# Kernel optimization log

Hardware: AMD Instinct MI355X
Metric: run time of the kernel (lower is better)

Reference implementation:

```python
import math
import jax, jax.numpy as jnp
import numpy as np

D_MODEL = 896
N_HEADS = 14
D_HEAD = D_MODEL // N_HEADS  # 64
ROPE_BASE = 10000.0
LN_EPS = 1e-5
B, N = 8, 1024


def setup_inputs() -> dict:
    key = jax.random.key(0)
    ks = jax.random.split(key, 12)
    s = 1.0 / math.sqrt(D_MODEL)
    return {
        "node_features": jax.random.normal(ks[0], (B, N, D_MODEL), jnp.float32),
        "adj": jax.random.uniform(ks[1], (N, N), jnp.float32),
        "wind_dirs": jax.random.uniform(ks[2], (B, N), jnp.float32),
        "bearings": jax.random.uniform(ks[3], (N, N), jnp.float32),
        "Wq": jax.random.normal(ks[4], (D_MODEL, D_MODEL), jnp.float32) * s,
        "Wk": jax.random.normal(ks[5], (D_MODEL, D_MODEL), jnp.float32) * s,
        "Wv": jax.random.normal(ks[6], (D_MODEL, D_MODEL), jnp.float32) * s,
        "Wo": jax.random.normal(ks[7], (D_MODEL, D_MODEL), jnp.float32) * s,
        "ln_g": jnp.ones((D_MODEL,), jnp.float32),
        "ln_b": jnp.zeros((D_MODEL,), jnp.float32),
        "wind_w": jax.random.normal(ks[8], (2, N_HEADS), jnp.float32) * (1.0 / math.sqrt(2.0)),
        "wind_b": jnp.zeros((N_HEADS,), jnp.float32),
    }


def _layernorm(x, g, b):
    mu = jnp.mean(x, axis=-1, keepdims=True)
    var = jnp.var(x, axis=-1, keepdims=True)
    return (x - mu) * jax.lax.rsqrt(var + LN_EPS) * g + b


def _apply_rotary(x, cos_h, sin_h):
    # x: (B,H,N,d_head); cos_h/sin_h: (N, d_head//2)
    d_half = x.shape[-1] // 2
    x1, x2 = x[..., :d_half], x[..., d_half:]
    return jnp.concatenate([x1 * cos_h - x2 * sin_h, x2 * cos_h + x1 * sin_h], axis=-1)


def reference(node_features, adj, wind_dirs, bearings, Wq, Wk, Wv, Wo, ln_g, ln_b, wind_w, wind_b):
    Bb, Nn, D = node_features.shape
    residual = node_features
    x = _layernorm(node_features, ln_g, ln_b)

    def proj(W):
        return (x @ W).reshape(Bb, Nn, N_HEADS, D_HEAD).transpose(0, 2, 1, 3)  # (B,H,N,dh)

    Q, K, V = proj(Wq), proj(Wk), proj(Wv)

    # RoPE: cos/sin halves (first d_half entries of the duplicated freq table)
    inv_freq = 1.0 / (ROPE_BASE ** (jnp.arange(0, D_HEAD, 2, dtype=jnp.float32) / D_HEAD))
    freqs = jnp.arange(Nn, dtype=jnp.float32)[:, None] * inv_freq[None, :]  # (N, dh/2)
    cos_h, sin_h = jnp.cos(freqs), jnp.sin(freqs)
    Q = _apply_rotary(Q, cos_h, sin_h)
    K = _apply_rotary(K, cos_h, sin_h)

    attn = jnp.einsum("bhqd,bhkd->bhqk", Q, K) / math.sqrt(D_HEAD)
    adj_mask = (adj > 0)[None, None, :, :]
    attn = jnp.where(adj_mask, attn, -1e30)

    # wind-direction dynamic edge bias
    reverse_bearings = (bearings.T + 180.0) % 360.0  # (N,N)
    alignment = jnp.cos(jnp.deg2rad(wind_dirs[:, :, None] - reverse_bearings[None]))  # (B,N,N)
    dist_feat = jnp.broadcast_to(adj[None], (Bb, Nn, Nn))
    edge_features = jnp.stack([alignment, dist_feat], axis=-1)  # (B,N,N,2)
    wind_bias = jnp.tanh(edge_features @ wind_w + wind_b)  # (B,N,N,H)
    attn = attn + wind_bias.transpose(0, 3, 1, 2)  # (B,H,N,N)

    attn = jax.nn.softmax(attn, axis=-1)  # dropout is identity in eval
    out = jnp.einsum("bhqk,bhkd->bhqd", attn, V)
    out = out.transpose(0, 2, 1, 3).reshape(Bb, Nn, D) @ Wo
    return residual + out
```

## Files before the change

kernel.cpp:

```cpp
#include <hip/hip_runtime.h>
#include <hip/hip_bf16.h>
#include <math.h>

#define B_ 8
#define N_ 1024
#define H_ 14
#define DH_ 64
#define D_ 896
#define M_ (B_*N_)
#define DQKV_ 2688

#define TWO_LOG2E_ 2.8853900817779268f
#define BIAS_C_   (-15.869645449778597f)
#define QSCALE_     0.18033688011112043f

typedef __attribute__((ext_vector_type(8))) short bf16x8;
typedef __attribute__((ext_vector_type(4))) short bf16x4;
typedef __attribute__((ext_vector_type(4))) float f32x4;
typedef __attribute__((ext_vector_type(4))) unsigned u32x4;

__device__ __forceinline__ float bf2f(short s){
  unsigned u = ((unsigned)(unsigned short)s) << 16;
  union { unsigned u; float f; } c; c.u = u; return c.f;
}
__device__ __forceinline__ short f2bf(float f){
  union { float f; unsigned u; } c; c.f = f;
  unsigned u = c.u;
  unsigned r = (u + 0x7FFFu + ((u >> 16) & 1u)) >> 16;
  return (short)(unsigned short)r;
}
__device__ __forceinline__ float asf(unsigned u){
  union { unsigned u; float f; } c; c.u = u; return c.f;
}

#define BAR_LDS() do { asm volatile("s_waitcnt lgkmcnt(0)" ::: "memory"); \
                       __builtin_amdgcn_s_barrier(); } while (0)

__global__ __launch_bounds__(256) void ln_kernel(const float* __restrict__ x,
                                                 const float* __restrict__ g,
                                                 const float* __restrict__ bb,
                                                 short* __restrict__ y)
{
  int row = blockIdx.x;
  const float* xr = x + (size_t)row * D_;
  float s = 0.f, s2 = 0.f;
  for (int i = threadIdx.x; i < D_; i += 256){
    float v = xr[i]; s += v; s2 = fmaf(v, v, s2);
  }
  #pragma unroll
  for (int off = 32; off > 0; off >>= 1){
    s  += __shfl_down(s,  off, 64);
    s2 += __shfl_down(s2, off, 64);
  }
  __shared__ float rs_[4], rs2_[4];
  int wv = threadIdx.x >> 6;
  if ((threadIdx.x & 63) == 0){ rs_[wv] = s; rs2_[wv] = s2; }
  __syncthreads();
  float ts  = rs_[0] + rs_[1] + rs_[2] + rs_[3];
  float ts2 = rs2_[0] + rs2_[1] + rs2_[2] + rs2_[3];
  float mu  = ts * (1.f / D_);
  float var = ts2 * (1.f / D_) - mu * mu;
  float rstd = rsqrtf(var + 1e-5f);
  short* yr = y + (size_t)row * D_;
  for (int i = threadIdx.x; i < D_; i += 256){
    yr[i] = f2bf((xr[i] - mu) * rstd * g[i] + bb[i]);
  }
}

__global__ __launch_bounds__(256) void transpose_kernel(
    const float* __restrict__ Wq, const float* __restrict__ Wk,
    const float* __restrict__ Wv, const float* __restrict__ Wo,
    short* __restrict__ WqkvT, short* __restrict__ WoT)
{
  __shared__ short t[64][72];
  int z = blockIdx.z;
  const float* W = (z == 0) ? Wq : (z == 1) ? Wk : (z == 2) ? Wv : Wo;
  int kb = blockIdx.x * 64, nb = blockIdx.y * 64;
  int c0 = (threadIdx.x & 7) * 8;
  int r0 = threadIdx.x >> 3;
  #pragma unroll
  for (int rr = 0; rr < 64; rr += 32){
    const float* src = &W[(size_t)(kb + r0 + rr) * D_ + nb + c0];
    float4 a = *(const float4*)src;
    float4 b = *(const float4*)(src + 4);
    short* dstl = &t[r0 + rr][c0];
    dstl[0] = f2bf(a.x); dstl[1] = f2bf(a.y); dstl[2] = f2bf(a.z); dstl[3] = f2bf(a.w);
    dstl[4] = f2bf(b.x); dstl[5] = f2bf(b.y); dstl[6] = f2bf(b.z); dstl[7] = f2bf(b.w);
  }
  __syncthreads();
  short* dst = (z < 3) ? (WqkvT + (size_t)(z * D_) * D_) : WoT;
  #pragma unroll
  for (int rr = 0; rr < 64; rr += 32){
    int n = nb + r0 + rr;
    bf16x8 v;
    #pragma unroll
    for (int j = 0; j < 8; j++) v[j] = t[c0 + j][r0 + rr];
    *(bf16x8*)&dst[(size_t)n * D_ + kb + c0] = v;
  }
}

__global__ __launch_bounds__(256) void prep_kernel(
    const float* __restrict__ adj, const float* __restrict__ brg,
    const float* __restrict__ wdir,
    unsigned* __restrict__ csb, short* __restrict__ adjT,
    short* __restrict__ alignT, int do_align)
{
  int kt = blockIdx.x, qt = blockIdx.y;
  __shared__ short tt[64][72];
  __shared__ float cA_[8][64], sA_[8][64];

  if (do_align){
    for (int idx = threadIdx.x; idx < 8 * 64; idx += 256){
      int b = idx >> 6, q = idx & 63;
      float A = wdir[(size_t)b * N_ + qt * 64 + q] * 0.017453292519943295f;
      float s, c; __sincosf(A, &s, &c);
      sA_[b][q] = s; cA_[b][q] = c;
    }
  }

  int r  = threadIdx.x >> 2;
  int c0 = (threadIdx.x & 3) * 16;

  {
    int q = qt * 64 + r;
    const float* ap = adj + (size_t)q * N_ + kt * 64 + c0;
    #pragma unroll
    for (int i = 0; i < 16; i += 4){
      float4 av = *(const float4*)(ap + i);
      tt[r][c0 + i]     = f2bf(av.x);
      tt[r][c0 + i + 1] = f2bf(av.y);
      tt[r][c0 + i + 2] = f2bf(av.z);
      tt[r][c0 + i + 3] = f2bf(av.w);
    }
  }
  __syncthreads();

  {
    int k = kt * 64 + r;
    const float* bp = brg + (size_t)k * N_ + qt * 64 + c0;
    unsigned* cp = csb + (size_t)k * N_ + qt * 64 + c0;
    #pragma unroll
    for (int i = 0; i < 16; i += 4){
      float4 bv = *(const float4*)(bp + i);
      float b4[4] = { bv.x, bv.y, bv.z, bv.w };
      float cB[4], sB[4];
      unsigned o[4];
      #pragma unroll
      for (int j = 0; j < 4; j++){
        float Br = (b4[j] + 180.f) * 0.017453292519943295f;
        __sincosf(Br, &sB[j], &cB[j]);
        o[j] = ((unsigned)(unsigned short)f2bf(cB[j])) |
               (((unsigned)(unsigned short)f2bf(sB[j])) << 16);
      }
      *(uint4*)(cp + i) = make_uint4(o[0], o[1], o[2], o[3]);
      if (do_align){
        #pragma unroll
        for (int b = 0; b < 8; b++){
          unsigned w2[2];
          #pragma unroll
          for (int p = 0; p < 2; p++){
            unsigned lo = 0, hi = 0;
            #pragma unroll
            for (int j = 0; j < 2; j++){
              int q = c0 + i + p * 2 + j;
              float al = fmaf(cA_[b][q], cB[p * 2 + j], sA_[b][q] * sB[p * 2 + j]);
              unsigned v = (unsigned)(unsigned short)f2bf(al);
              if (j == 0) lo = v; else hi = v;
            }
            w2[p] = lo | (hi << 16);
          }
          *(uint2*)(alignT + ((size_t)b * N_ + k) * N_ + qt * 64 + c0 + i) =
              make_uint2(w2[0], w2[1]);
        }
      }
    }
  }

  {
    int k = kt * 64 + r;
    short* op = adjT + (size_t)k * N_ + qt * 64 + c0;
    bf16x8 v0, v1;
    #pragma unroll
    for (int j = 0; j < 8; j++){ v0[j] = tt[c0 + j][r]; v1[j] = tt[c0 + 8 + j][r]; }
    *(bf16x8*)op = v0;
    *(bf16x8*)(op + 8) = v1;
  }
}

__global__ __launch_bounds__(256) void gemm_bt(const short* __restrict__ A,
                                               const short* __restrict__ Bt,
                                               short* __restrict__ C,
                                               float* __restrict__ Cf,
                                               const float* __restrict__ residf,
                                               int N, int rope)
{
  const int K = D_;
  __shared__ short As[128 * 32];
  __shared__ short Bs[128 * 32];
  int tid  = threadIdx.x;
  int wave = tid >> 6;
  int lane = tid & 63;
  int quad = lane >> 4;
  int l16  = lane & 15;
  int wr = wave >> 1, wc = wave & 1;
  int m0 = blockIdx.x * 128;
  int n0 = blockIdx.y * 128;

  f32x4 acc[4][4];
  #pragma unroll
  for (int i = 0; i < 4; i++)
    #pragma unroll
    for (int j = 0; j < 4; j++)
      acc[i][j] = (f32x4){0.f, 0.f, 0.f, 0.f};

  for (int k0 = 0; k0 < K; k0 += 32){
    __syncthreads();
    #pragma unroll
    for (int it = 0; it < 2; ++it){
      int c   = tid + it * 256;
      int row = c >> 2;
      int cc  = c & 3;
      const short* ga = A  + (size_t)(m0 + row) * K + k0 + cc * 8;
      const short* gb = Bt + (size_t)(n0 + row) * K + k0 + cc * 8;
      short* la = As + (size_t)(wave * 64 + it * 256) * 8;
      short* lb = Bs + (size_t)(wave * 64 + it * 256) * 8;
      __builtin_amdgcn_global_load_lds((const __attribute__((address_space(1))) void*)ga,
                                       (__attribute__((address_space(3))) void*)la, 16, 0, 0);
      __builtin_amdgcn_global_load_lds((const __attribute__((address_space(1))) void*)gb,
                                       (__attribute__((address_space(3))) void*)lb, 16, 0, 0);
    }
    __syncthreads();

    bf16x8 af[4], bfr[4];
    #pragma unroll
    for (int i = 0; i < 4; i++)
      af[i] = *(const bf16x8*)(As + (size_t)(wr * 64 + i * 16 + l16) * 32 + quad * 8);
    #pragma unroll
    for (int j = 0; j < 4; j++)
      bfr[j] = *(const bf16x8*)(Bs + (size_t)(wc * 64 + j * 16 + l16) * 32 + quad * 8);
    #pragma unroll
    for (int i = 0; i < 4; i++)
      #pragma unroll
      for (int j = 0; j < 4; j++)
        acc[i][j] = __builtin_amdgcn_mfma_f32_16x16x32_bf16(af[i], bfr[j], acc[i][j], 0, 0, 0);
  }

  if (rope){
    int cb  = n0 + wc * 64;
    int mat = cb / D_;
    if (mat < 2){
      float scale = (mat == 0) ? QSCALE_ : 1.0f;
      float invf0 = exp2f(-0.4152410118609203f * (float)l16);
      float invf1 = invf0 * 0.01f;
      #pragma unroll
      for (int i = 0; i < 4; i++){
        #pragma unroll
        for (int rr = 0; rr < 4; rr++){
          int r = m0 + wr * 64 + i * 16 + quad * 4 + rr;
          float nseq = (float)(r & (N_ - 1));
          float s0, c0v, s1, c1v;
          __sincosf(nseq * invf0, &s0, &c0v);
          __sincosf(nseq * invf1, &s1, &c1v);
          float x1 = acc[i][0][rr], x2 = acc[i][2][rr];
          acc[i][0][rr] = (x1 * c0v - x2 * s0) * scale;
          acc[i][2][rr] = (x2 * c0v + x1 * s0) * scale;
          x1 = acc[i][1][rr]; x2 = acc[i][3][rr];
          acc[i][1][rr] = (x1 * c1v - x2 * s1) * scale;
          acc[i][3][rr] = (x2 * c1v + x1 * s1) * scale;
        }
      }
    }
  }

  #pragma unroll
  for (int i = 0; i < 4; i++){
    #pragma unroll
    for (int rr = 0; rr < 4; rr++){
      int r = m0 + wr * 64 + i * 16 + quad * 4 + rr;
      size_t rowoff = (size_t)r * N;
      #pragma unroll
      for (int j = 0; j < 4; j++){
        int cidx = n0 + wc * 64 + j * 16 + l16;
        float v = acc[i][j][rr];
        if (Cf){
          Cf[rowoff + cidx] = v + residf[rowoff + cidx];
        } else {
          C[rowoff + cidx] = f2bf(v);
        }
      }
    }
  }
}

template<int PRE>
__global__ __launch_bounds__(512, 4) void attn_kernel(
    const short* __restrict__ QKV,
    const unsigned* __restrict__ csb,
    const short* __restrict__ adjT,
    const short* __restrict__ alignT,
    const float* __restrict__ wind_dirs,
    const float* __restrict__ wind_w,
    const float* __restrict__ wind_b,
    short* __restrict__ outb)
{
  __shared__ short K_s[64 * 72];
  __shared__ short V_t[64 * 76];
  __shared__ short P_s[128 * 76];

  int bid = blockIdx.x;
  int qt  = bid & 7;
  int hh  = (bid >> 3) % H_;
  int b   = bid / (8 * H_);
  int q0  = qt * 128;

  int t    = threadIdx.x;
  int w    = t >> 6;
  int lane = t & 63;
  int quad = lane >> 4;
  int l16  = lane & 15;

  const short* qp = QKV + ((size_t)(b * N_) + q0 + w * 16 + l16) * DQKV_ + hh * DH_;
  bf16x8 qf0 = *(const bf16x8*)(qp + quad * 8);
  bf16x8 qf1 = *(const bf16x8*)(qp + 32 + quad * 8);

  float cA[4], sA[4];
  if (!PRE){
    #pragma unroll
    for (int rr = 0; rr < 4; rr++){
      float wd = wind_dirs[(size_t)b * N_ + q0 + w * 16 + quad * 4 + rr];
      float A  = wd * 0.017453292519943295f;
      sA[rr] = __sinf(A);
      cA[rr] = __cosf(A);
    }
  }
  float w0m = wind_w[hh]      * TWO_LOG2E_;
  float w1m = wind_w[H_ + hh] * TWO_LOG2E_;
  float wbm = wind_b[hh]      * TWO_LOG2E_;

  float l[4] = {0.f, 0.f, 0.f, 0.f};
  f32x4 O[4];
  #pragma unroll
  for (int dc = 0; dc < 4; dc++) O[dc] = (f32x4){0.f, 0.f, 0.f, 0.f};

  int kr  = t >> 3, kc8 = (t & 7) * 8;
  int vk2 = (t >> 4) * 2, vd4 = (t & 15) * 4;
  const short* kg0 = QKV + ((size_t)(b * N_) + kr)  * DQKV_ + D_     + hh * DH_ + kc8;
  const short* vg0 = QKV + ((size_t)(b * N_) + vk2) * DQKV_ + 2 * D_ + hh * DH_ + vd4;

  bf16x8 pk  = *(const bf16x8*)kg0;
  bf16x4 pv0 = *(const bf16x4*)vg0;
  bf16x4 pv1 = *(const bf16x4*)(vg0 + DQKV_);

  size_t bias_q = (size_t)(q0 + w * 16 + quad * 4);
  u32x4 cs4a[4]; bf16x4 al4a[4]; bf16x4 av4a[4];
  #pragma unroll
  for (int jc = 0; jc < 4; jc++){
    size_t off = (size_t)(jc * 16 + l16) * N_ + bias_q;
    if (PRE) al4a[jc] = *(const bf16x4*)(alignT + (size_t)b * N_ * N_ + off);
    else     cs4a[jc] = *(const u32x4*)(csb + off);
    av4a[jc] = *(const bf16x4*)(adjT + off);
  }

  for (int kt = 0; kt < 16; ++kt){
    int k0 = kt * 64;
    BAR_LDS();
    *(bf16x8*)(K_s + kr * 72 + kc8) = pk;
    #pragma unroll
    for (int j = 0; j < 4; j++){
      unsigned pv = ((unsigned)(unsigned short)pv0[j]) |
                    (((unsigned)(unsigned short)pv1[j]) << 16);
      *(unsigned*)(V_t + (vd4 + j) * 76 + vk2) = pv;
    }
    BAR_LDS();

    int kn = (kt < 15) ? (k0 + 64) : k0;
    pk  = *(const bf16x8*)(kg0 + (size_t)kn * DQKV_);
    pv0 = *(const bf16x4*)(vg0 + (size_t)kn * DQKV_);
    pv1 = *(const bf16x4*)(vg0 + (size_t)(kn + 1) * DQKV_);

    f32x4 S[4];
    __builtin_amdgcn_s_setprio(1);
    #pragma unroll
    for (int jc = 0; jc < 4; jc++){
      S[jc] = (f32x4){0.f, 0.f, 0.f, 0.f};
      bf16x8 kf0 = *(const bf16x8*)(K_s + (jc * 16 + l16) * 72 + quad * 8);
      bf16x8 kf1 = *(const bf16x8*)(K_s + (jc * 16 + l16) * 72 + 32 + quad * 8);
      S[jc] = __builtin_amdgcn_mfma_f32_16x16x32_bf16(qf0, kf0, S[jc], 0, 0, 0);
      S[jc] = __builtin_amdgcn_mfma_f32_16x16x32_bf16(qf1, kf1, S[jc], 0, 0, 0);
    }
    __builtin_amdgcn_s_setprio(0);

    #pragma unroll
    for (int jc = 0; jc < 4; jc++){
      #pragma unroll
      for (int rr = 0; rr < 4; rr++){
        float av = bf2f(av4a[jc][rr]);
        float align;
        if (PRE){
          align = bf2f(al4a[jc][rr]);
        } else {
          unsigned u = cs4a[jc][rr];
          float cB = asf(u << 16);
          float sB = asf(u & 0xffff0000u);
          align = cA[rr] * cB + sA[rr] * sB;
        }
        float z2 = fmaf(align, w0m, fmaf(av, w1m, wbm));
        float e2 = __builtin_amdgcn_exp2f(z2);
        float rc = __builtin_amdgcn_rcpf(e2 + 1.f);
        float bias2 = fmaf(-TWO_LOG2E_, rc, BIAS_C_);
        float sv = (av > 0.f ? S[jc][rr] : -1e30f) + bias2;
        float e = __builtin_amdgcn_exp2f(sv);
        l[rr] += e;
        P_s[(w * 16 + quad * 4 + rr) * 76 + jc * 16 + l16] = f2bf(e);
      }
    }

    #pragma unroll
    for (int jc = 0; jc < 4; jc++){
      size_t off = (size_t)(kn + jc * 16 + l16) * N_ + bias_q;
      if (PRE) al4a[jc] = *(const bf16x4*)(alignT + (size_t)b * N_ * N_ + off);
      else     cs4a[jc] = *(const u32x4*)(csb + off);
      av4a[jc] = *(const bf16x4*)(adjT + off);
    }

    __builtin_amdgcn_s_setprio(1);
    #pragma unroll
    for (int kc = 0; kc < 2; kc++){
      const short* pp = P_s + (w * 16 + l16) * 76 + kc * 32 + quad * 8;
      bf16x4 p0 = *(const bf16x4*)pp;
      bf16x4 p1 = *(const bf16x4*)(pp + 4);
      bf16x8 pf = { p0[0], p0[1], p0[2], p0[3], p1[0], p1[1], p1[2], p1[3] };
      #pragma unroll
      for (int dc = 0; dc < 4; dc++){
        const short* vp = V_t + (dc * 16 + l16) * 76 + kc * 32 + quad * 8;
        bf16x4 u0 = *(const bf16x4*)vp;
        bf16x4 u1 = *(const bf16x4*)(vp + 4);
        bf16x8 vf = { u0[0], u0[1], u0[2], u0[3], u1[0], u1[1], u1[2], u1[3] };
        O[dc] = __builtin_amdgcn_mfma_f32_16x16x32_bf16(pf, vf, O[dc], 0, 0, 0);
      }
    }
    __builtin_amdgcn_s_setprio(0);
  }

  float rl[4];
  #pragma unroll
  for (int rr = 0; rr < 4; rr++){
    float rs = l[rr];
    rs += __shfl_xor(rs, 1);
    rs += __shfl_xor(rs, 2);
    rs += __shfl_xor(rs, 4);
    rs += __shfl_xor(rs, 8);
    rl[rr] = 1.f / rs;
  }
  short* op = outb + ((size_t)(b * N_) + q0 + w * 16) * D_ + hh * DH_;
  #pragma unroll
  for (int rr = 0; rr < 4; rr++)
    #pragma unroll
    for (int dc = 0; dc < 4; dc++)
      op[(size_t)(quad * 4 + rr) * D_ + dc * 16 + l16] = f2bf(O[dc][rr] * rl[rr]);
}

extern "C" void kernel_launch(void* const* d_in, const int* in_sizes, int n_in,
                              void* d_out, int out_size, void* d_ws, size_t ws_size,
                              hipStream_t stream)
{
  const float* nf   = (const float*)d_in[0];
  const float* adj  = (const float*)d_in[1];
  const float* wdir = (const float*)d_in[2];
  const float* brg  = (const float*)d_in[3];
  const float* Wq   = (const float*)d_in[4];
  const float* Wk   = (const float*)d_in[5];
  const float* Wv   = (const float*)d_in[6];
  const float* Wo   = (const float*)d_in[7];
  const float* lng  = (const float*)d_in[8];
  const float* lnb  = (const float*)d_in[9];
  const float* ww   = (const float*)d_in[10];
  const float* wbb  = (const float*)d_in[11];
  float* out = (float*)d_out;

  short* base = (short*)d_ws;
  size_t sh = 0;
  short* xln   = base + sh;  sh += (size_t)M_ * D_;
  short* WqkvT = base + sh;  sh += (size_t)DQKV_ * D_;
  short* WoT   = base + sh;  sh += (size_t)D_ * D_;
  short* QKV   = base + sh;  sh += (size_t)M_ * DQKV_;
  unsigned* csb = (unsigned*)(base + sh); sh += (size_t)N_ * N_ * 2;
  short* adjT  = base + sh;  sh += (size_t)N_ * N_;
  short* alignT = base + sh; sh += (size_t)B_ * N_ * N_;
  size_t need_pre = sh * sizeof(short);
  bool pre = (ws_size >= need_pre);

  ln_kernel<<<M_, 256, 0, stream>>>(nf, lng, lnb, xln);
  transpose_kernel<<<dim3(14, 14, 4), 256, 0, stream>>>(Wq, Wk, Wv, Wo, WqkvT, WoT);
  prep_kernel<<<dim3(16, 16), 256, 0, stream>>>(adj, brg, wdir, csb, adjT, alignT, pre ? 1 : 0);
  gemm_bt<<<dim3(M_ / 128, DQKV_ / 128), 256, 0, stream>>>(xln, WqkvT, QKV, nullptr, nullptr, DQKV_, 1);
  if (pre)
    attn_kernel<1><<<B_ * H_ * 8, 512, 0, stream>>>(QKV, csb, adjT, alignT, wdir, ww, wbb, xln);
  else
    attn_kernel<0><<<B_ * H_ * 8, 512, 0, stream>>>(QKV, csb, adjT, alignT, wdir, ww, wbb, xln);
  gemm_bt<<<dim3(M_ / 128, D_ / 128), 256, 0, stream>>>(xln, WoT, nullptr, out, nf, D_, 0);
}
```

Measured before the change: 388.9 us.

## Reorder attention grid, stagger key-tile start, interleave softmax with PV MFMA

```diff
diff --git a/kernel.cpp b/kernel.cpp
--- a/kernel.cpp
+++ b/kernel.cpp
@@ -31,6 +31,11 @@
 }
 __device__ __forceinline__ float asf(unsigned u){
   union { unsigned u; float f; } c; c.u = u; return c.f;
+}
+__device__ __forceinline__ unsigned cvt_pk_bf16(float lo, float hi){
+  unsigned r;
+  asm("v_cvt_pk_bf16_f32 %0, %1, %2" : "=v"(r) : "v"(lo), "v"(hi));
+  return r;
 }
 
 #define BAR_LDS() do { asm volatile("s_waitcnt lgkmcnt(0)" ::: "memory"); \
@@ -308,10 +313,12 @@
   __shared__ short P_s[128 * 76];
 
   int bid = blockIdx.x;
-  int qt  = bid & 7;
-  int hh  = (bid >> 3) % H_;
-  int b   = bid / (8 * H_);
+  int qt  = bid / 112;
+  int rem = bid - qt * 112;
+  int hh  = rem >> 3;
+  int b   = rem & 7;
   int q0  = qt * 128;
+  int kt0 = (qt * 2) & 15;
 
   int t    = threadIdx.x;
   int w    = t >> 6;
@@ -347,22 +354,25 @@
   const short* kg0 = QKV + ((size_t)(b * N_) + kr)  * DQKV_ + D_     + hh * DH_ + kc8;
   const short* vg0 = QKV + ((size_t)(b * N_) + vk2) * DQKV_ + 2 * D_ + hh * DH_ + vd4;
 
-  bf16x8 pk  = *(const bf16x8*)kg0;
-  bf16x4 pv0 = *(const bf16x4*)vg0;
-  bf16x4 pv1 = *(const bf16x4*)(vg0 + DQKV_);
+  int k0f = kt0 * 64;
+  bf16x8 pk  = *(const bf16x8*)(kg0 + (size_t)k0f * DQKV_);
+  bf16x4 pv0 = *(const bf16x4*)(vg0 + (size_t)k0f * DQKV_);
+  bf16x4 pv1 = *(const bf16x4*)(vg0 + (size_t)(k0f + 1) * DQKV_);
 
   size_t bias_q = (size_t)(q0 + w * 16 + quad * 4);
   u32x4 cs4a[4]; bf16x4 al4a[4]; bf16x4 av4a[4];
   #pragma unroll
   for (int jc = 0; jc < 4; jc++){
-    size_t off = (size_t)(jc * 16 + l16) * N_ + bias_q;
+    size_t off = (size_t)(k0f + jc * 16 + l16) * N_ + bias_q;
     if (PRE) al4a[jc] = *(const bf16x4*)(alignT + (size_t)b * N_ * N_ + off);
     else     cs4a[jc] = *(const u32x4*)(csb + off);
     av4a[jc] = *(const bf16x4*)(adjT + off);
   }
 
-  for (int kt = 0; kt < 16; ++kt){
-    int k0 = kt * 64;
+  for (int it = 0; it < 16; ++it){
+    int ktn = (it + 1 + kt0) & 15;
+    int kn  = ktn * 64;
+
     BAR_LDS();
     *(bf16x8*)(K_s + kr * 72 + kc8) = pk;
     #pragma unroll
@@ -373,7 +383,6 @@
     }
     BAR_LDS();
 
-    int kn = (kt < 15) ? (k0 + 64) : k0;
     pk  = *(const bf16x8*)(kg0 + (size_t)kn * DQKV_);
     pv0 = *(const bf16x4*)(vg0 + (size_t)kn * DQKV_);
     pv1 = *(const bf16x4*)(vg0 + (size_t)(kn + 1) * DQKV_);
@@ -391,55 +400,65 @@
     __builtin_amdgcn_s_setprio(0);
 
     #pragma unroll
-    for (int jc = 0; jc < 4; jc++){
+    for (int kc = 0; kc < 2; kc++){
       #pragma unroll
-      for (int rr = 0; rr < 4; rr++){
-        float av = bf2f(av4a[jc][rr]);
-        float align;
-        if (PRE){
-          align = bf2f(al4a[jc][rr]);
-        } else {
-          unsigned u = cs4a[jc][rr];
-          float cB = asf(u << 16);
-          float sB = asf(u & 0xffff0000u);
-          align = cA[rr] * cB + sA[rr] * sB;
+      for (int jc = kc * 2; jc < kc * 2 + 2; jc++){
+        float ev[4];
+        #pragma unroll
+        for (int rr = 0; rr < 4; rr++){
+          float av = bf2f(av4a[jc][rr]);
+          float align;
+          if (PRE){
+            align = bf2f(al4a[jc][rr]);
+          } else {
+            unsigned u = cs4a[jc][rr];
+            float cB = asf(u << 16);
+            float sB = asf(u & 0xffff0000u);
+            align = cA[rr] * cB + sA[rr] * sB;
+          }
+          float z2 = fmaf(align, w0m, fmaf(av, w1m, wbm));
+          float e2 = __builtin_amdgcn_exp2f(z2);
+          float rc = __builtin_amdgcn_rcpf(e2 + 1.f);
+          float bias2 = fmaf(-TWO_LOG2E_, rc, BIAS_C_);
+          float sv = (av > 0.f ? S[jc][rr] : -1e30f) + bias2;
+          float e = __builtin_amdgcn_exp2f(sv);
+          l[rr] += e;
+          ev[rr] = e;
         }
-        float z2 = fmaf(align, w0m, fmaf(av, w1m, wbm));
-        float e2 = __builtin_amdgcn_exp2f(z2);
-        float rc = __builtin_amdgcn_rcpf(e2 + 1.f);
-        float bias2 = fmaf(-TWO_LOG2E_, rc, BIAS_C_);
-        float sv = (av > 0.f ? S[jc][rr] : -1e30f) + bias2;
-        float e = __builtin_amdgcn_exp2f(sv);
-        l[rr] += e;
-        P_s[(w * 16 + quad * 4 + rr) * 76 + jc * 16 + l16] = f2bf(e);
-      }
-    }
-
-    #pragma unroll
-    for (int jc = 0; jc < 4; jc++){
-      size_t off = (size_t)(kn + jc * 16 + l16) * N_ + bias_q;
-      if (PRE) al4a[jc] = *(const bf16x4*)(alignT + (size_t)b * N_ * N_ + off);
-      else     cs4a[jc] = *(const u32x4*)(csb + off);
-      av4a[jc] = *(const bf16x4*)(adjT + off);
-    }
-
-    __builtin_amdgcn_s_setprio(1);
-    #pragma unroll
-    for (int kc = 0; kc < 2; kc++){
-      const short* pp = P_s + (w * 16 + l16) * 76 + kc * 32 + quad * 8;
-      bf16x4 p0 = *(const bf16x4*)pp;
-      bf16x4 p1 = *(const bf16x4*)(pp + 4);
-      bf16x8 pf = { p0[0], p0[1], p0[2], p0[3], p1[0], p1[1], p1[2], p1[3] };
+        unsigned pk01 = cvt_pk_bf16(ev[0], ev[1]);
+        unsigned pk23 = cvt_pk_bf16(ev[2], ev[3]);
+        short* pb = P_s + (w * 16 + quad * 4) * 76 + jc * 16 + l16;
+        pb[0]   = (short)pk01;
+        pb[76]  = (short)(pk01 >> 16);
+        pb[152] = (short)pk23;
+        pb[228] = (short)(pk23 >> 16);
+      }
+
+      __builtin_amdgcn_s_setprio(1);
+      {
+        const short* pp = P_s + (w * 16 + l16) * 76 + kc * 32 + quad * 8;
+        bf16x4 p0 = *(const bf16x4*)pp;
+        bf16x4 p1 = *(const bf16x4*)(pp + 4);
+        bf16x8 pf = { p0[0], p0[1], p0[2], p0[3], p1[0], p1[1], p1[2], p1[3] };
+        #pragma unroll
+        for (int dc = 0; dc < 4; dc++){
+          const short* vp = V_t + (dc * 16 + l16) * 76 + kc * 32 + quad * 8;
+          bf16x4 u0 = *(const bf16x4*)vp;
+          bf16x4 u1 = *(const bf16x4*)(vp + 4);
+          bf16x8 vf = { u0[0], u0[1], u0[2], u0[3], u1[0], u1[1], u1[2], u1[3] };
+          O[dc] = __builtin_amdgcn_mfma_f32_16x16x32_bf16(pf, vf, O[dc], 0, 0, 0);
+        }
+      }
+      __builtin_amdgcn_s_setprio(0);
+
       #pragma unroll
-      for (int dc = 0; dc < 4; dc++){
-        const short* vp = V_t + (dc * 16 + l16) * 76 + kc * 32 + quad * 8;
-        bf16x4 u0 = *(const bf16x4*)vp;
-        bf16x4 u1 = *(const bf16x4*)(vp + 4);
-        bf16x8 vf = { u0[0], u0[1], u0[2], u0[3], u1[0], u1[1], u1[2], u1[3] };
-        O[dc] = __builtin_amdgcn_mfma_f32_16x16x32_bf16(pf, vf, O[dc], 0, 0, 0);
-      }
-    }
-    __builtin_amdgcn_s_setprio(0);
+      for (int jc = kc * 2; jc < kc * 2 + 2; jc++){
+        size_t off = (size_t)(kn + jc * 16 + l16) * N_ + bias_q;
+        if (PRE) al4a[jc] = *(const bf16x4*)(alignT + (size_t)b * N_ * N_ + off);
+        else     cs4a[jc] = *(const u32x4*)(csb + off);
+        av4a[jc] = *(const bf16x4*)(adjT + off);
+      }
+    }
   }
 
   float rl[4];
```

Result: no change. 384.4 us (-1.2%).
